# Performance work log

Hardware: AMD Instinct MI355X
Metric: run time of the kernel (lower is better)

Reference implementation:

```python
import jax, jax.numpy as jnp
import numpy as np

N = 50000      # nodes in frontier (degree-bucketed batch)
N_CH = 5       # max_output_degree / children per node
X = 256        # x_size
H = 256        # h_size


def setup_inputs() -> dict:
    key = jax.random.key(0)
    ks = jax.random.split(key, 8)
    s = 0.05  # param scale
    return {
        "x": jax.random.normal(ks[0], (N, X), dtype=jnp.float32),
        "x_mask": jnp.ones((N,), dtype=jnp.float32),
        "neighbour_h": jax.random.normal(ks[1], (N, N_CH, H), dtype=jnp.float32),
        "neighbour_c": jax.random.normal(ks[2], (N, N_CH, H), dtype=jnp.float32),
        "W_iou_in": jax.random.normal(ks[3], (X, 3 * H), dtype=jnp.float32) * s,
        "b_iou_in": jnp.zeros((3 * H,), dtype=jnp.float32),
        "W_f_in": jax.random.normal(ks[4], (X, H), dtype=jnp.float32) * s,
        "b_f_in": jnp.zeros((H,), dtype=jnp.float32),
        "W_aggr_iou": jax.random.normal(ks[5], (N_CH * H, 3 * H), dtype=jnp.float32) * s,
        "b_aggr_iou": jnp.zeros((3 * H,), dtype=jnp.float32),
        "W_aggr_f": jax.random.normal(ks[6], (N_CH * H, N_CH * H), dtype=jnp.float32) * s,
        "b_aggr_f": jnp.zeros((N_CH * H,), dtype=jnp.float32),
    }


def reference(x, x_mask, neighbour_h, neighbour_c,
              W_iou_in, b_iou_in, W_f_in, b_f_in,
              W_aggr_iou, b_aggr_iou, W_aggr_f, b_aggr_f):
    n_batch = neighbour_h.shape[0]
    n_ch = neighbour_h.shape[1]
    h_flat = neighbour_h.reshape(n_batch, n_ch * H)  # [N, n_ch*H]

    # forget gates (note: source adds f_input twice -- reproduced faithfully)
    f_input = (x @ W_f_in + b_f_in) * x_mask[:, None]          # [N, H]
    f_input = jnp.tile(f_input, (1, n_ch))                      # [N, n_ch*H]
    f_gate = h_flat @ W_aggr_f + b_aggr_f + f_input             # forget_module + f_input
    f_aggr = f_gate + f_input                                   # + f_input again (as in source)

    # iou aggregation over children
    iou_aggr = h_flat @ W_aggr_iou + b_aggr_iou                  # [N, 3H]

    f = jax.nn.sigmoid(f_aggr).reshape(n_batch, n_ch, H)
    c_aggr = jnp.sum(f * neighbour_c, axis=1)                    # [N, H]

    # apply_node_func
    iou = (x @ W_iou_in + b_iou_in) * x_mask[:, None] + iou_aggr
    i, o, u = jnp.split(iou, 3, axis=1)
    i, o, u = jax.nn.sigmoid(i), jax.nn.sigmoid(o), jnp.tanh(u)
    c = i * u + c_aggr
    h = o * jnp.tanh(c)
    return h, c
```

## Files before the change

### kernel.cpp

```cpp
#include <hip/hip_runtime.h>
#include <hip/hip_bf16.h>

typedef __bf16 bf16x8 __attribute__((ext_vector_type(8)));
typedef float floatx4 __attribute__((ext_vector_type(4)));

#define GLOBAL_AS __attribute__((address_space(1)))
#define LDS_AS __attribute__((address_space(3)))

constexpr int M_NODES = 50000;
constexpr int HSZ  = 256;
constexpr int KDIM = 1536;
constexpr int NDIM = 2048;
constexpr int BM = 128, BN = 256, BK = 64;
constexpr int MT = (M_NODES + BM - 1) / BM;
constexpr int NT = NDIM / BN;
constexpr size_t WCT_BYTES = (size_t)NDIM * KDIM * 2;
constexpr size_t A_BYTES   = (size_t)M_NODES * KDIM * 2;

__global__ __launch_bounds__(256) void prep_weights(
    const float* __restrict__ W_iou_in, const float* __restrict__ W_f_in,
    const float* __restrict__ W_aggr_iou, const float* __restrict__ W_aggr_f,
    __bf16* __restrict__ WcT)
{
  int idx = blockIdx.x * 256 + threadIdx.x;
  if (idx >= NDIM * KDIM) return;
  int n = idx / KDIM, k = idx - n * KDIM;
  int tb = n >> 8;
  int u  = (n >> 7) & 1;
  int s  = (n >> 4) & 7;
  int tl = n & 15;
  int t  = tb * 32 + u * 16 + tl;
  float v;
  if (k < 256) {
    if (s < 5) v = 2.0f * W_f_in[k * 256 + t];
    else       v = W_iou_in[k * 768 + (s - 5) * 256 + t];
  } else {
    int kh = k - 256;
    if (s < 5) v = W_aggr_f[kh * 1280 + s * 256 + t];
    else       v = W_aggr_iou[kh * 768 + (s - 5) * 256 + t];
  }
  WcT[idx] = (__bf16)v;
}

__global__ __launch_bounds__(256) void prep_A(
    const float* __restrict__ x, const float* __restrict__ xmask,
    const float* __restrict__ nh, __bf16* __restrict__ Abf)
{
  int ci = blockIdx.x * 256 + threadIdx.x;
  if (ci >= M_NODES * (KDIM / 8)) return;
  int row = ci / (KDIM / 8);
  int kc  = ci - row * (KDIM / 8);
  const float* src;
  float sc;
  if (kc < 32) { src = x  + (size_t)row * 256  + kc * 8;        sc = xmask[row]; }
  else         { src = nh + (size_t)row * 1280 + (size_t)(kc - 32) * 8; sc = 1.0f; }
  float4 f0 = *(const float4*)src;
  float4 f1 = *(const float4*)(src + 4);
  bf16x8 v;
  v[0] = (__bf16)(f0.x * sc); v[1] = (__bf16)(f0.y * sc);
  v[2] = (__bf16)(f0.z * sc); v[3] = (__bf16)(f0.w * sc);
  v[4] = (__bf16)(f1.x * sc); v[5] = (__bf16)(f1.y * sc);
  v[6] = (__bf16)(f1.z * sc); v[7] = (__bf16)(f1.w * sc);
  *(bf16x8*)(Abf + (size_t)row * KDIM + kc * 8) = v;
}

__device__ __forceinline__ float sigm(float v) {
  return __builtin_amdgcn_rcpf(1.0f + __expf(-v));
}
__device__ __forceinline__ float tanh_(float v) {
  return 2.0f * __builtin_amdgcn_rcpf(1.0f + __expf(-2.0f * v)) - 1.0f;
}

template <bool FROM_ABF>
__global__ __launch_bounds__(256, 2) void gemm_treelstm2(
    const __bf16* __restrict__ Abf, const __bf16* __restrict__ WcT,
    const float* __restrict__ x, const float* __restrict__ xmask,
    const float* __restrict__ nh, const float* __restrict__ nc,
    const float* __restrict__ b_iou, const float* __restrict__ b_f,
    const float* __restrict__ b_aiou, const float* __restrict__ b_af,
    float* __restrict__ out)
{
  __shared__ __bf16 ldsA[BM * BK];
  __shared__ __bf16 ldsB[BN * BK];

  const int bid  = blockIdx.x;
  const int wgid = (bid & 7) * (MT * NT / 8) + (bid >> 3);
  const int bn   = wgid & 7;
  const int m0   = (wgid >> 3) * BM;

  const int tid  = threadIdx.x;
  const int lane = tid & 63;
  const int w    = tid >> 6;
  const int wr   = w >> 1, wc = w & 1;
  const int frow = lane & 15, kq = lane >> 4;
  const int l8   = lane >> 3, pch = lane & 7;

  const __bf16* pA[4];
  const __bf16* pB[8];
  const float* xp[4]; const float* nhp[4]; float am[4]; int ac[4]; int arl[4];
#pragma unroll
  for (int j = 0; j < 4; ++j) {
    const int rl = w * 32 + j * 8 + l8;
    const int c  = pch ^ (rl & 7);
    int gr = m0 + rl; if (gr >= M_NODES) gr = M_NODES - 1;
    if constexpr (FROM_ABF) {
      pA[j] = Abf + (size_t)gr * KDIM + c * 8;
    } else {
      arl[j] = rl; ac[j] = c;
      xp[j]  = x  + (size_t)gr * 256;
      nhp[j] = nh + (size_t)gr * 1280 - 256;
      am[j]  = xmask[gr];
    }
  }
#pragma unroll
  for (int j = 0; j < 8; ++j) {
    const int rl = w * 64 + j * 8 + l8;
    const int c  = pch ^ (rl & 7);
    pB[j] = WcT + (size_t)(bn * BN + rl) * KDIM + c * 8;
  }

  int aoff[4][2], boff[8][2];
#pragma unroll
  for (int mf = 0; mf < 4; ++mf) {
    const int ra = wr * 64 + mf * 16 + frow;
#pragma unroll
    for (int ks = 0; ks < 2; ++ks)
      aoff[mf][ks] = ra * BK + (((ks * 4 + kq) ^ (ra & 7)) * 8);
  }
#pragma unroll
  for (int nf = 0; nf < 8; ++nf) {
    const int rb = wc * 128 + nf * 16 + frow;
#pragma unroll
    for (int ks = 0; ks < 2; ++ks)
      boff[nf][ks] = rb * BK + (((ks * 4 + kq) ^ (rb & 7)) * 8);
  }

  floatx4 acc[4][8];
#pragma unroll
  for (int i = 0; i < 4; ++i)
#pragma unroll
    for (int j = 0; j < 8; ++j) acc[i][j] = (floatx4)(0.0f);

  for (int kt = 0; kt < KDIM / BK; ++kt) {
    __syncthreads();
    if constexpr (FROM_ABF) {
#pragma unroll
      for (int j = 0; j < 4; ++j) {
        __builtin_amdgcn_global_load_lds((const GLOBAL_AS void*)pA[j],
            (LDS_AS void*)((LDS_AS char*)(LDS_AS __bf16*)ldsA + (w * 32 + j * 8) * 128), 16, 0, 0);
        pA[j] += BK;
      }
#pragma unroll
      for (int j = 0; j < 8; ++j) {
        __builtin_amdgcn_global_load_lds((const GLOBAL_AS void*)pB[j],
            (LDS_AS void*)((LDS_AS char*)(LDS_AS __bf16*)ldsB + (w * 64 + j * 8) * 128), 16, 0, 0);
        pB[j] += BK;
      }
    } else {
      const int k0base = kt * BK;
#pragma unroll
      for (int j = 0; j < 4; ++j) {
        const int k0 = k0base + ac[j] * 8;
        const float* src = (k0 < 256) ? (xp[j] + k0) : (nhp[j] + k0);
        const float sc   = (k0 < 256) ? am[j] : 1.0f;
        float4 f0 = *(const float4*)src;
        float4 f1 = *(const float4*)(src + 4);
        bf16x8 v;
        v[0] = (__bf16)(f0.x * sc); v[1] = (__bf16)(f0.y * sc);
        v[2] = (__bf16)(f0.z * sc); v[3] = (__bf16)(f0.w * sc);
        v[4] = (__bf16)(f1.x * sc); v[5] = (__bf16)(f1.y * sc);
        v[6] = (__bf16)(f1.z * sc); v[7] = (__bf16)(f1.w * sc);
        *(bf16x8*)&ldsA[arl[j] * BK + pch * 8] = v;
      }
#pragma unroll
      for (int j = 0; j < 8; ++j) {
        bf16x8 vb = *(const bf16x8*)pB[j];
        *(bf16x8*)&ldsB[(w * 64 + j * 8 + l8) * BK + pch * 8] = vb;
        pB[j] += BK;
      }
    }
    __syncthreads();

#pragma unroll
    for (int ks = 0; ks < 2; ++ks) {
      bf16x8 a0 = *(const bf16x8*)&ldsA[aoff[0][ks]];
      bf16x8 a1 = *(const bf16x8*)&ldsA[aoff[1][ks]];
      bf16x8 a2 = *(const bf16x8*)&ldsA[aoff[2][ks]];
      bf16x8 a3 = *(const bf16x8*)&ldsA[aoff[3][ks]];
#pragma unroll
      for (int nf = 0; nf < 8; ++nf) {
        bf16x8 b = *(const bf16x8*)&ldsB[boff[nf][ks]];
        acc[0][nf] = __builtin_amdgcn_mfma_f32_16x16x32_bf16(a0, b, acc[0][nf], 0, 0, 0);
        acc[1][nf] = __builtin_amdgcn_mfma_f32_16x16x32_bf16(a1, b, acc[1][nf], 0, 0, 0);
        acc[2][nf] = __builtin_amdgcn_mfma_f32_16x16x32_bf16(a2, b, acc[2][nf], 0, 0, 0);
        acc[3][nf] = __builtin_amdgcn_mfma_f32_16x16x32_bf16(a3, b, acc[3][nf], 0, 0, 0);
      }
    }
  }

  const int t = bn * 32 + wc * 16 + frow;
  float baf5[5];
#pragma unroll
  for (int s = 0; s < 5; ++s) baf5[s] = b_af[s * 256 + t];
  const float bf2 = 2.0f * b_f[t];
  float biou3[3], baiou3[3];
#pragma unroll
  for (int g = 0; g < 3; ++g) {
    biou3[g]  = b_iou[g * 256 + t];
    baiou3[g] = b_aiou[g * 256 + t];
  }

#pragma unroll
  for (int mf = 0; mf < 4; ++mf) {
#pragma unroll
    for (int j = 0; j < 4; ++j) {
      const int r = m0 + wr * 64 + mf * 16 + kq * 4 + j;
      if (r >= M_NODES) continue;
      const float mk = xmask[r];
      float ca = 0.0f;
#pragma unroll
      for (int s = 0; s < 5; ++s) {
        const float fa = acc[mf][s][j] + baf5[s] + mk * bf2;
        ca += sigm(fa) * nc[((size_t)r * 5 + s) * 256 + t];
      }
      const float iv = sigm(acc[mf][5][j] + mk * biou3[0] + baiou3[0]);
      const float ov = sigm(acc[mf][6][j] + mk * biou3[1] + baiou3[1]);
      const float uv = tanh_(acc[mf][7][j] + mk * biou3[2] + baiou3[2]);
      const float c  = iv * uv + ca;
      const float h  = ov * tanh_(c);
      out[(size_t)r * HSZ + t] = h;
      out[(size_t)M_NODES * HSZ + (size_t)r * HSZ + t] = c;
    }
  }
}

extern "C" void kernel_launch(void* const* d_in, const int* in_sizes, int n_in,
                              void* d_out, int out_size, void* d_ws, size_t ws_size,
                              hipStream_t stream)
{
  const float* x      = (const float*)d_in[0];
  const float* xmask  = (const float*)d_in[1];
  const float* nh     = (const float*)d_in[2];
  const float* nc     = (const float*)d_in[3];
  const float* W_iou  = (const float*)d_in[4];
  const float* b_iou  = (const float*)d_in[5];
  const float* W_f    = (const float*)d_in[6];
  const float* b_f    = (const float*)d_in[7];
  const float* W_aiou = (const float*)d_in[8];
  const float* b_aiou = (const float*)d_in[9];
  const float* W_af   = (const float*)d_in[10];
  const float* b_af   = (const float*)d_in[11];
  __bf16* WcT = (__bf16*)d_ws;
  float* out  = (float*)d_out;

  prep_weights<<<(NDIM * KDIM + 255) / 256, 256, 0, stream>>>(W_iou, W_f, W_aiou, W_af, WcT);

  if (ws_size >= WCT_BYTES + A_BYTES) {
    __bf16* Abf = (__bf16*)((char*)d_ws + WCT_BYTES);
    prep_A<<<(M_NODES * (KDIM / 8) + 255) / 256, 256, 0, stream>>>(x, xmask, nh, Abf);
    gemm_treelstm2<true><<<dim3(MT * NT), 256, 0, stream>>>(
        Abf, WcT, x, xmask, nh, nc, b_iou, b_f, b_aiou, b_af, out);
  } else {
    gemm_treelstm2<false><<<dim3(MT * NT), 256, 0, stream>>>(
        nullptr, WcT, x, xmask, nh, nc, b_iou, b_f, b_aiou, b_af, out);
  }
}
```

Before: 920.8 us.

## Add triple-buffered 256x256 MFMA GEMM with eight waves and phased barriers

```diff
diff --git a/kernel.cpp b/kernel.cpp
--- a/kernel.cpp
+++ b/kernel.cpp
@@ -11,11 +11,15 @@
 constexpr int HSZ  = 256;
 constexpr int KDIM = 1536;
 constexpr int NDIM = 2048;
-constexpr int BM = 128, BN = 256, BK = 64;
+constexpr size_t WCT_BYTES = (size_t)NDIM * KDIM * 2;
+constexpr size_t A_BYTES   = (size_t)M_NODES * KDIM * 2;
+
+constexpr int BM = 256, BN = 256, BK = 32;
 constexpr int MT = (M_NODES + BM - 1) / BM;
 constexpr int NT = NDIM / BN;
-constexpr size_t WCT_BYTES = (size_t)NDIM * KDIM * 2;
-constexpr size_t A_BYTES   = (size_t)M_NODES * KDIM * 2;
+constexpr int NKT = KDIM / BK;
+constexpr int SLOT  = BM * BK * 2 + BN * BK * 2;
+constexpr int BOFF0 = BM * BK * 2;
 
 __global__ __launch_bounds__(256) void prep_weights(
     const float* __restrict__ W_iou_in, const float* __restrict__ W_f_in,
@@ -71,22 +75,165 @@
   return 2.0f * __builtin_amdgcn_rcpf(1.0f + __expf(-2.0f * v)) - 1.0f;
 }
 
-template <bool FROM_ABF>
-__global__ __launch_bounds__(256, 2) void gemm_treelstm2(
+__global__ __launch_bounds__(512, 2) void gemm_8ph(
     const __bf16* __restrict__ Abf, const __bf16* __restrict__ WcT,
+    const float* __restrict__ xmask, const float* __restrict__ nc,
+    const float* __restrict__ b_iou, const float* __restrict__ b_f,
+    const float* __restrict__ b_aiou, const float* __restrict__ b_af,
+    float* __restrict__ out)
+{
+  __shared__ __attribute__((aligned(128))) char lds[3 * SLOT];
+
+  const int bid  = blockIdx.x;
+  const int wgid = (bid & 7) * (MT * NT / 8) + (bid >> 3);
+  const int bn   = wgid & 7;
+  const int m0   = (wgid >> 3) * BM;
+
+  const int tid  = threadIdx.x;
+  const int lane = tid & 63;
+  const int w    = tid >> 6;
+  const int wr   = w >> 1;
+  const int wc   = w & 1;
+  const int frow = lane & 15, kq = lane >> 4;
+
+  const int srow = lane >> 2;
+  const int sch  = (lane & 3) ^ (srow & 3);
+  int arL = m0 + w * 16 + srow;        if (arL >= M_NODES) arL = M_NODES - 1;
+  int arH = m0 + 128 + w * 16 + srow;  if (arH >= M_NODES) arH = M_NODES - 1;
+  const __bf16* pAL = Abf + (size_t)arL * KDIM + sch * 8;
+  const __bf16* pAH = Abf + (size_t)arH * KDIM + sch * 8;
+  const __bf16* pBL = WcT + (size_t)(bn * BN + w * 16 + srow) * KDIM + sch * 8;
+  const __bf16* pBH = WcT + (size_t)(bn * BN + 128 + w * 16 + srow) * KDIM + sch * 8;
+  LDS_AS char* ldsb = (LDS_AS char*)lds;
+  const int dAL = w * 1024;
+  const int dAH = 8192 + w * 1024;
+  const int dBL = BOFF0 + w * 1024;
+  const int dBH = BOFF0 + 8192 + w * 1024;
+
+  const int swz = (kq ^ (frow & 3)) << 4;
+  int aoff[4], boff[8];
+#pragma unroll
+  for (int mf = 0; mf < 4; ++mf) aoff[mf] = (wr * 64 + mf * 16 + frow) * 64 + swz;
+#pragma unroll
+  for (int nf = 0; nf < 8; ++nf) boff[nf] = BOFF0 + (wc * 128 + nf * 16 + frow) * 64 + swz;
+
+  floatx4 acc[4][8];
+#pragma unroll
+  for (int i = 0; i < 4; ++i)
+#pragma unroll
+    for (int j = 0; j < 8; ++j) acc[i][j] = (floatx4)(0.0f);
+
+#define STAGE_LO(koff, sl) do { \
+    __builtin_amdgcn_global_load_lds((const GLOBAL_AS void*)(pAL + (koff)), \
+        (LDS_AS void*)(ldsb + (sl) + dAL), 16, 0, 0); \
+    __builtin_amdgcn_global_load_lds((const GLOBAL_AS void*)(pBL + (koff)), \
+        (LDS_AS void*)(ldsb + (sl) + dBL), 16, 0, 0); \
+  } while (0)
+#define STAGE_HI(koff, sl) do { \
+    __builtin_amdgcn_global_load_lds((const GLOBAL_AS void*)(pAH + (koff)), \
+        (LDS_AS void*)(ldsb + (sl) + dAH), 16, 0, 0); \
+    __builtin_amdgcn_global_load_lds((const GLOBAL_AS void*)(pBH + (koff)), \
+        (LDS_AS void*)(ldsb + (sl) + dBH), 16, 0, 0); \
+  } while (0)
+
+  STAGE_LO(0, 0);        STAGE_HI(0, 0);
+  STAGE_LO(BK, SLOT);    STAGE_HI(BK, SLOT);
+
+  int slotC = 0, slotN = SLOT, slotT = 2 * SLOT;
+  for (int kt = 0; kt < NKT; ++kt) {
+    const int kS = (kt + 2 < NKT ? kt + 2 : NKT - 1) * BK;
+    asm volatile("s_waitcnt vmcnt(4)" ::: "memory");
+    __builtin_amdgcn_s_barrier();
+    asm volatile("" ::: "memory");
+
+    bf16x8 b[8];
+#pragma unroll
+    for (int nf = 0; nf < 8; ++nf) b[nf] = *(const bf16x8*)(lds + slotC + boff[nf]);
+    bf16x8 a0 = *(const bf16x8*)(lds + slotC + aoff[0]);
+    bf16x8 a1 = *(const bf16x8*)(lds + slotC + aoff[1]);
+    STAGE_LO(kS, slotT);
+    __builtin_amdgcn_s_setprio(1);
+#pragma unroll
+    for (int nf = 0; nf < 8; ++nf) {
+      acc[0][nf] = __builtin_amdgcn_mfma_f32_16x16x32_bf16(a0, b[nf], acc[0][nf], 0, 0, 0);
+      acc[1][nf] = __builtin_amdgcn_mfma_f32_16x16x32_bf16(a1, b[nf], acc[1][nf], 0, 0, 0);
+    }
+    __builtin_amdgcn_s_setprio(0);
+    __builtin_amdgcn_sched_barrier(0);
+    __builtin_amdgcn_s_barrier();
+    asm volatile("" ::: "memory");
+
+    bf16x8 a2 = *(const bf16x8*)(lds + slotC + aoff[2]);
+    bf16x8 a3 = *(const bf16x8*)(lds + slotC + aoff[3]);
+    STAGE_HI(kS, slotT);
+    __builtin_amdgcn_s_setprio(1);
+#pragma unroll
+    for (int nf = 0; nf < 8; ++nf) {
+      acc[2][nf] = __builtin_amdgcn_mfma_f32_16x16x32_bf16(a2, b[nf], acc[2][nf], 0, 0, 0);
+      acc[3][nf] = __builtin_amdgcn_mfma_f32_16x16x32_bf16(a3, b[nf], acc[3][nf], 0, 0, 0);
+    }
+    __builtin_amdgcn_s_setprio(0);
+    __builtin_amdgcn_sched_barrier(0);
+
+    int t0 = slotC; slotC = slotN; slotN = slotT; slotT = t0;
+  }
+#undef STAGE_LO
+#undef STAGE_HI
+
+  const int t = bn * 32 + wc * 16 + frow;
+  float baf5[5];
+#pragma unroll
+  for (int s = 0; s < 5; ++s) baf5[s] = b_af[s * 256 + t];
+  const float bf2 = 2.0f * b_f[t];
+  float biou3[3], baiou3[3];
+#pragma unroll
+  for (int g = 0; g < 3; ++g) {
+    biou3[g]  = b_iou[g * 256 + t];
+    baiou3[g] = b_aiou[g * 256 + t];
+  }
+
+#pragma unroll
+  for (int mf = 0; mf < 4; ++mf) {
+#pragma unroll
+    for (int j = 0; j < 4; ++j) {
+      const int r = m0 + wr * 64 + mf * 16 + kq * 4 + j;
+      if (r >= M_NODES) continue;
+      const float mk = xmask[r];
+      float ca = 0.0f;
+#pragma unroll
+      for (int s = 0; s < 5; ++s) {
+        const float fa = acc[mf][s][j] + baf5[s] + mk * bf2;
+        ca += sigm(fa) * nc[((size_t)r * 5 + s) * 256 + t];
+      }
+      const float iv = sigm(acc[mf][5][j] + mk * biou3[0] + baiou3[0]);
+      const float ov = sigm(acc[mf][6][j] + mk * biou3[1] + baiou3[1]);
+      const float uv = tanh_(acc[mf][7][j] + mk * biou3[2] + baiou3[2]);
+      const float c  = iv * uv + ca;
+      const float h  = ov * tanh_(c);
+      out[(size_t)r * HSZ + t] = h;
+      out[(size_t)M_NODES * HSZ + (size_t)r * HSZ + t] = c;
+    }
+  }
+}
+
+constexpr int FBM = 128, FBN = 256, FBK = 64;
+constexpr int FMT = (M_NODES + FBM - 1) / FBM;
+constexpr int FNT = NDIM / FBN;
+__global__ __launch_bounds__(256, 2) void gemm_fb(
+    const __bf16* __restrict__ WcT,
     const float* __restrict__ x, const float* __restrict__ xmask,
     const float* __restrict__ nh, const float* __restrict__ nc,
     const float* __restrict__ b_iou, const float* __restrict__ b_f,
     const float* __restrict__ b_aiou, const float* __restrict__ b_af,
     float* __restrict__ out)
 {
-  __shared__ __bf16 ldsA[BM * BK];
-  __shared__ __bf16 ldsB[BN * BK];
+  __shared__ __bf16 ldsA[FBM * FBK];
+  __shared__ __bf16 ldsB[FBN * FBK];
 
   const int bid  = blockIdx.x;
-  const int wgid = (bid & 7) * (MT * NT / 8) + (bid >> 3);
+  const int wgid = (bid & 7) * (FMT * FNT / 8) + (bid >> 3);
   const int bn   = wgid & 7;
-  const int m0   = (wgid >> 3) * BM;
+  const int m0   = (wgid >> 3) * FBM;
 
   const int tid  = threadIdx.x;
   const int lane = tid & 63;
@@ -95,7 +242,6 @@
   const int frow = lane & 15, kq = lane >> 4;
   const int l8   = lane >> 3, pch = lane & 7;
 
-  const __bf16* pA[4];
   const __bf16* pB[8];
   const float* xp[4]; const float* nhp[4]; float am[4]; int ac[4]; int arl[4];
 #pragma unroll
@@ -103,20 +249,16 @@
     const int rl = w * 32 + j * 8 + l8;
     const int c  = pch ^ (rl & 7);
     int gr = m0 + rl; if (gr >= M_NODES) gr = M_NODES - 1;
-    if constexpr (FROM_ABF) {
-      pA[j] = Abf + (size_t)gr * KDIM + c * 8;
-    } else {
-      arl[j] = rl; ac[j] = c;
-      xp[j]  = x  + (size_t)gr * 256;
-      nhp[j] = nh + (size_t)gr * 1280 - 256;
-      am[j]  = xmask[gr];
-    }
+    arl[j] = rl; ac[j] = c;
+    xp[j]  = x  + (size_t)gr * 256;
+    nhp[j] = nh + (size_t)gr * 1280 - 256;
+    am[j]  = xmask[gr];
   }
 #pragma unroll
   for (int j = 0; j < 8; ++j) {
     const int rl = w * 64 + j * 8 + l8;
     const int c  = pch ^ (rl & 7);
-    pB[j] = WcT + (size_t)(bn * BN + rl) * KDIM + c * 8;
+    pB[j] = WcT + (size_t)(bn * FBN + rl) * KDIM + c * 8;
   }
 
   int aoff[4][2], boff[8][2];
@@ -125,14 +267,14 @@
     const int ra = wr * 64 + mf * 16 + frow;
 #pragma unroll
     for (int ks = 0; ks < 2; ++ks)
-      aoff[mf][ks] = ra * BK + (((ks * 4 + kq) ^ (ra & 7)) * 8);
+      aoff[mf][ks] = ra * FBK + (((ks * 4 + kq) ^ (ra & 7)) * 8);
   }
 #pragma unroll
   for (int nf = 0; nf < 8; ++nf) {
     const int rb = wc * 128 + nf * 16 + frow;
 #pragma unroll
     for (int ks = 0; ks < 2; ++ks)
-      boff[nf][ks] = rb * BK + (((ks * 4 + kq) ^ (rb & 7)) * 8);
+      boff[nf][ks] = rb * FBK + (((ks * 4 + kq) ^ (rb & 7)) * 8);
   }
 
   floatx4 acc[4][8];
@@ -141,46 +283,30 @@
 #pragma unroll
     for (int j = 0; j < 8; ++j) acc[i][j] = (floatx4)(0.0f);
 
-  for (int kt = 0; kt < KDIM / BK; ++kt) {
+  for (int kt = 0; kt < KDIM / FBK; ++kt) {
     __syncthreads();
-    if constexpr (FROM_ABF) {
-#pragma unroll
-      for (int j = 0; j < 4; ++j) {
-        __builtin_amdgcn_global_load_lds((const GLOBAL_AS void*)pA[j],
-            (LDS_AS void*)((LDS_AS char*)(LDS_AS __bf16*)ldsA + (w * 32 + j * 8) * 128), 16, 0, 0);
-        pA[j] += BK;
-      }
-#pragma unroll
-      for (int j = 0; j < 8; ++j) {
-        __builtin_amdgcn_global_load_lds((const GLOBAL_AS void*)pB[j],
-            (LDS_AS void*)((LDS_AS char*)(LDS_AS __bf16*)ldsB + (w * 64 + j * 8) * 128), 16, 0, 0);
-        pB[j] += BK;
-      }
-    } else {
-      const int k0base = kt * BK;
-#pragma unroll
-      for (int j = 0; j < 4; ++j) {
-        const int k0 = k0base + ac[j] * 8;
-        const float* src = (k0 < 256) ? (xp[j] + k0) : (nhp[j] + k0);
-        const float sc   = (k0 < 256) ? am[j] : 1.0f;
-        float4 f0 = *(const float4*)src;
-        float4 f1 = *(const float4*)(src + 4);
-        bf16x8 v;
-        v[0] = (__bf16)(f0.x * sc); v[1] = (__bf16)(f0.y * sc);
-        v[2] = (__bf16)(f0.z * sc); v[3] = (__bf16)(f0.w * sc);
-        v[4] = (__bf16)(f1.x * sc); v[5] = (__bf16)(f1.y * sc);
-        v[6] = (__bf16)(f1.z * sc); v[7] = (__bf16)(f1.w * sc);
-        *(bf16x8*)&ldsA[arl[j] * BK + pch * 8] = v;
-      }
-#pragma unroll
-      for (int j = 0; j < 8; ++j) {
-        bf16x8 vb = *(const bf16x8*)pB[j];
-        *(bf16x8*)&ldsB[(w * 64 + j * 8 + l8) * BK + pch * 8] = vb;
-        pB[j] += BK;
-      }
+    const int k0base = kt * FBK;
+#pragma unroll
+    for (int j = 0; j < 4; ++j) {
+      const int k0 = k0base + ac[j] * 8;
+      const float* src = (k0 < 256) ? (xp[j] + k0) : (nhp[j] + k0);
+      const float sc   = (k0 < 256) ? am[j] : 1.0f;
+      float4 f0 = *(const float4*)(src);
+      float4 f1 = *(const float4*)(src + 4);
+      bf16x8 v;
+      v[0] = (__bf16)(f0.x * sc); v[1] = (__bf16)(f0.y * sc);
+      v[2] = (__bf16)(f0.z * sc); v[3] = (__bf16)(f0.w * sc);
+      v[4] = (__bf16)(f1.x * sc); v[5] = (__bf16)(f1.y * sc);
+      v[6] = (__bf16)(f1.z * sc); v[7] = (__bf16)(f1.w * sc);
+      *(bf16x8*)&ldsA[arl[j] * FBK + pch * 8] = v;
+    }
+#pragma unroll
+    for (int j = 0; j < 8; ++j) {
+      bf16x8 vb = *(const bf16x8*)pB[j];
+      *(bf16x8*)&ldsB[(w * 64 + j * 8 + l8) * FBK + pch * 8] = vb;
+      pB[j] += FBK;
     }
     __syncthreads();
-
 #pragma unroll
     for (int ks = 0; ks < 2; ++ks) {
       bf16x8 a0 = *(const bf16x8*)&ldsA[aoff[0][ks]];
@@ -189,11 +315,11 @@
       bf16x8 a3 = *(const bf16x8*)&ldsA[aoff[3][ks]];
 #pragma unroll
       for (int nf = 0; nf < 8; ++nf) {
-        bf16x8 b = *(const bf16x8*)&ldsB[boff[nf][ks]];
-        acc[0][nf] = __builtin_amdgcn_mfma_f32_16x16x32_bf16(a0, b, acc[0][nf], 0, 0, 0);
-        acc[1][nf] = __builtin_amdgcn_mfma_f32_16x16x32_bf16(a1, b, acc[1][nf], 0, 0, 0);
-        acc[2][nf] = __builtin_amdgcn_mfma_f32_16x16x32_bf16(a2, b, acc[2][nf], 0, 0, 0);
-        acc[3][nf] = __builtin_amdgcn_mfma_f32_16x16x32_bf16(a3, b, acc[3][nf], 0, 0, 0);
+        bf16x8 bb = *(const bf16x8*)&ldsB[boff[nf][ks]];
+        acc[0][nf] = __builtin_amdgcn_mfma_f32_16x16x32_bf16(a0, bb, acc[0][nf], 0, 0, 0);
+        acc[1][nf] = __builtin_amdgcn_mfma_f32_16x16x32_bf16(a1, bb, acc[1][nf], 0, 0, 0);
+        acc[2][nf] = __builtin_amdgcn_mfma_f32_16x16x32_bf16(a2, bb, acc[2][nf], 0, 0, 0);
+        acc[3][nf] = __builtin_amdgcn_mfma_f32_16x16x32_bf16(a3, bb, acc[3][nf], 0, 0, 0);
       }
     }
   }
@@ -209,7 +335,6 @@
     biou3[g]  = b_iou[g * 256 + t];
     baiou3[g] = b_aiou[g * 256 + t];
   }
-
 #pragma unroll
   for (int mf = 0; mf < 4; ++mf) {
 #pragma unroll
@@ -258,10 +383,10 @@
   if (ws_size >= WCT_BYTES + A_BYTES) {
     __bf16* Abf = (__bf16*)((char*)d_ws + WCT_BYTES);
     prep_A<<<(M_NODES * (KDIM / 8) + 255) / 256, 256, 0, stream>>>(x, xmask, nh, Abf);
-    gemm_treelstm2<true><<<dim3(MT * NT), 256, 0, stream>>>(
-        Abf, WcT, x, xmask, nh, nc, b_iou, b_f, b_aiou, b_af, out);
+    gemm_8ph<<<dim3(MT * NT), 512, 0, stream>>>(
+        Abf, WcT, xmask, nc, b_iou, b_f, b_aiou, b_af, out);
   } else {
-    gemm_treelstm2<false><<<dim3(MT * NT), 256, 0, stream>>>(
-        nullptr, WcT, x, xmask, nh, nc, b_iou, b_f, b_aiou, b_af, out);
-  }
-}
+    gemm_fb<<<dim3(FMT * FNT), 256, 0, stream>>>(
+        WcT, x, xmask, nh, nc, b_iou, b_f, b_aiou, b_af, out);
+  }
+}
```

Result: no change. 907.4 us (-1.4%).
